# Performance work log

Measured on AMD Instinct MI355X. Metric: run time of the kernel, lower is better.

The kernel has to match this reference:

```python
import jax, jax.numpy as jnp
import numpy as np

S = 4  # HMM states
# allowed transitions among the 4 recurrent states (plus self-loops);
# the (0,4) edge targets a terminal state outside the recurrent block and is omitted
_allow = np.zeros((S, S), dtype=bool)
for i, j in [(0, 0), (1, 1), (2, 2), (3, 3), (0, 1), (1, 2), (2, 3), (0, 2), (1, 3)]:
    _allow[i, j] = True
MASK = jnp.asarray(_allow)
NEG = -1e9


def setup_inputs() -> dict:
    key = jax.random.key(0)
    k0, k1, k2, k3, k4 = jax.random.split(key, 5)
    return {
        "x": jax.random.normal(k0, (256, 4096, 26), dtype=jnp.float32),
        "emit_logits": jax.random.normal(k1, (S, 26), dtype=jnp.float32) * 0.3,
        "trans_logits": jax.random.normal(k2, (S, S), dtype=jnp.float32) * 0.3,
        "init_logits": jax.random.normal(k3, (S,), dtype=jnp.float32) * 0.3,
        "w_out": jax.random.normal(k4, (1, S, 5), dtype=jnp.float32) * 0.3,
    }


def _posterior(x, emit_logits, trans_logits, init_logits):
    # x: [B,T,A] logits -> softmax over alphabet (as in call())
    p = jax.nn.softmax(x, axis=-1)                       # [B,T,A]
    Bmat = jax.nn.softmax(emit_logits, axis=-1)          # [S,A] emission distributions
    # expected emission likelihood per state, in log space
    log_emit = jnp.log(jnp.einsum('bta,sa->bts', p, Bmat) + 1e-16)  # [B,T,S]

    neg = jnp.asarray(NEG, x.dtype)
    logA = jax.nn.log_softmax(jnp.where(MASK, trans_logits, neg), axis=-1)
    logA = jnp.where(MASK, logA, neg)                    # [S,S]
    log_pi = jax.nn.log_softmax(init_logits)             # [S]

    le = jnp.moveaxis(log_emit, 1, 0)                    # [T,B,S]
    T = le.shape[0]

    # forward recursion: alpha_t = e_t + LSE_prev(alpha_{t-1} + logA)
    a0 = log_pi[None, :] + le[0]                         # [B,S]
    def fstep(carry, e):
        nc = e + jax.nn.logsumexp(carry[:, :, None] + logA[None], axis=1)
        return nc, nc
    _, alphas = jax.lax.scan(fstep, a0, le[1:])
    alphas = jnp.concatenate([a0[None], alphas], axis=0)  # [T,B,S]

    # backward recursion: beta_t = LSE_next(logA + e_{t+1} + beta_{t+1})
    bT = jnp.zeros_like(a0)
    def bstep(carry, e_next):
        nc = jax.nn.logsumexp(logA[None] + (e_next + carry)[:, None, :], axis=2)
        return nc, nc
    _, betas = jax.lax.scan(bstep, bT, le[1:], reverse=True)
    betas = jnp.concatenate([betas, bT[None]], axis=0)    # [T,B,S]

    gamma = jax.nn.softmax(alphas + betas, axis=-1)       # posterior [T,B,S]
    return jnp.moveaxis(gamma, 0, 1)[:, :, None, :]       # [B,T,1,S]


def reference(x, emit_logits, trans_logits, init_logits, w_out):
    gamma = _posterior(x, emit_logits, trans_logits, init_logits)  # [B,T,1,S]
    return jnp.einsum('bthd,hdo->bto', gamma, w_out)               # [B,T,5]
```

## Files before the change

### kernel.cpp

```cpp
#include <hip/hip_runtime.h>

#define TDIM 4096
#define BDIM 256
#define ADIM 26
#define SDIM 4
#define NEGF -1e30f
#define LOG2E 1.44269504088896340736f

__device__ __forceinline__ float ex2(float x) { return __builtin_amdgcn_exp2f(x); }
__device__ __forceinline__ float lg2(float x) { return __builtin_amdgcn_logf(x); }

__device__ __forceinline__ float l2se2(float a, float b) {
    float mx = fmaxf(a, b), mn = fminf(a, b);
    return mx + lg2(1.f + ex2(mn - mx));
}
__device__ __forceinline__ float l2se3(float a, float b, float c) {
    float mx = fmaxf(fmaxf(a, b), c);
    float md = __builtin_amdgcn_fmed3f(a, b, c);
    float mn = fminf(fminf(a, b), c);
    return mx + lg2(1.f + ex2(md - mx) + ex2(mn - mx));
}
__device__ __forceinline__ float l2se4(float a, float b, float c, float d) {
    float h1 = fmaxf(a, b), l1 = fminf(a, b);
    float h2 = fmaxf(c, d), l2 = fminf(c, d);
    float mx = fmaxf(h1, h2), s2 = fminf(h1, h2);
    return mx + lg2(1.f + ex2(s2 - mx) + ex2(l1 - mx) + ex2(l2 - mx));
}

struct TransA { float A00, A01, A02, A11, A12, A13, A22, A23, A33; };

__device__ __forceinline__ TransA make_transA(const float* __restrict__ trans) {
    TransA A;
    {
        float l0 = trans[0], l1 = trans[1], l2 = trans[2];
        float m = fmaxf(fmaxf(l0, l1), l2);
        float lz = m + __logf(__expf(l0 - m) + __expf(l1 - m) + __expf(l2 - m));
        A.A00 = (l0 - lz) * LOG2E; A.A01 = (l1 - lz) * LOG2E; A.A02 = (l2 - lz) * LOG2E;
    }
    {
        float l1 = trans[5], l2 = trans[6], l3 = trans[7];
        float m = fmaxf(fmaxf(l1, l2), l3);
        float lz = m + __logf(__expf(l1 - m) + __expf(l2 - m) + __expf(l3 - m));
        A.A11 = (l1 - lz) * LOG2E; A.A12 = (l2 - lz) * LOG2E; A.A13 = (l3 - lz) * LOG2E;
    }
    {
        float l2 = trans[10], l3 = trans[11];
        float m = fmaxf(l2, l3);
        float lz = m + __logf(__expf(l2 - m) + __expf(l3 - m));
        A.A22 = (l2 - lz) * LOG2E; A.A23 = (l3 - lz) * LOG2E;
    }
    A.A33 = 0.f;
    return A;
}

struct UT { float m00, m01, m02, m03, m11, m12, m13, m22, m23, m33; };

__device__ __forceinline__ void fstep(UT& M, const TransA& A, float4 e) {
    float n00 = M.m00 + A.A00 + e.x;
    float n01 = l2se2(M.m00 + A.A01, M.m01 + A.A11) + e.y;
    float n02 = l2se3(M.m00 + A.A02, M.m01 + A.A12, M.m02 + A.A22) + e.z;
    float n03 = l2se3(M.m01 + A.A13, M.m02 + A.A23, M.m03) + e.w;
    float n11 = M.m11 + A.A11 + e.y;
    float n12 = l2se2(M.m11 + A.A12, M.m12 + A.A22) + e.z;
    float n13 = l2se3(M.m11 + A.A13, M.m12 + A.A23, M.m13) + e.w;
    float n22 = M.m22 + A.A22 + e.z;
    float n23 = l2se2(M.m22 + A.A23, M.m23) + e.w;
    float n33 = M.m33 + e.w;
    M.m00 = n00; M.m01 = n01; M.m02 = n02; M.m03 = n03;
    M.m11 = n11; M.m12 = n12; M.m13 = n13; M.m22 = n22; M.m23 = n23; M.m33 = n33;
}

__device__ __forceinline__ UT ut_compose(const UT& A, const UT& B) {
    UT C;
    C.m00 = A.m00 + B.m00;
    C.m01 = l2se2(A.m00 + B.m01, A.m01 + B.m11);
    C.m02 = l2se3(A.m00 + B.m02, A.m01 + B.m12, A.m02 + B.m22);
    C.m03 = l2se4(A.m00 + B.m03, A.m01 + B.m13, A.m02 + B.m23, A.m03 + B.m33);
    C.m11 = A.m11 + B.m11;
    C.m12 = l2se2(A.m11 + B.m12, A.m12 + B.m22);
    C.m13 = l2se3(A.m11 + B.m13, A.m12 + B.m23, A.m13 + B.m33);
    C.m22 = A.m22 + B.m22;
    C.m23 = l2se2(A.m22 + B.m23, A.m23 + B.m33);
    C.m33 = A.m33 + B.m33;
    return C;
}

__device__ __forceinline__ void ut_renorm(UT& M) {
    float m1 = fmaxf(fmaxf(M.m00, M.m01), fmaxf(M.m02, M.m03));
    float m2 = fmaxf(fmaxf(M.m11, M.m12), fmaxf(M.m13, M.m22));
    float m3 = fmaxf(M.m23, M.m33);
    float mx = fmaxf(fmaxf(m1, m2), m3);
    M.m00 -= mx; M.m01 -= mx; M.m02 -= mx; M.m03 -= mx;
    M.m11 -= mx; M.m12 -= mx; M.m13 -= mx; M.m22 -= mx; M.m23 -= mx; M.m33 -= mx;
}

__device__ __forceinline__ void ut_store11(float* p, const UT& M) {
    p[0] = M.m00; p[1] = M.m01; p[2] = M.m02; p[3] = M.m03;
    p[4] = M.m11; p[5] = M.m12; p[6] = M.m13;
    p[7] = M.m22; p[8] = M.m23; p[9] = M.m33;
}
__device__ __forceinline__ UT ut_load11(const float* p) {
    UT M;
    M.m00 = p[0]; M.m01 = p[1]; M.m02 = p[2]; M.m03 = p[3];
    M.m11 = p[4]; M.m12 = p[5]; M.m13 = p[6];
    M.m22 = p[7]; M.m23 = p[8]; M.m33 = p[9];
    return M;
}

__device__ __forceinline__ void vecmat(float& v0, float& v1, float& v2, float& v3,
                                       const float* m) {
    float n0 = v0 + m[0];
    float n1 = l2se2(v0 + m[1], v1 + m[4]);
    float n2 = l2se3(v0 + m[2], v1 + m[5], v2 + m[7]);
    float n3 = l2se4(v0 + m[3], v1 + m[6], v2 + m[8], v3 + m[9]);
    float mm = fmaxf(fmaxf(n0, n1), fmaxf(n2, n3));
    v0 = n0 - mm; v1 = n1 - mm; v2 = n2 - mm; v3 = n3 - mm;
}
__device__ __forceinline__ void matvec(const float* m,
                                       float& u0, float& u1, float& u2, float& u3) {
    float n0 = l2se4(m[0] + u0, m[1] + u1, m[2] + u2, m[3] + u3);
    float n1 = l2se3(m[4] + u1, m[5] + u2, m[6] + u3);
    float n2 = l2se2(m[7] + u2, m[8] + u3);
    float n3 = m[9] + u3;
    float mm = fmaxf(fmaxf(n0, n1), fmaxf(n2, n3));
    u0 = n0 - mm; u1 = n1 - mm; u2 = n2 - mm; u3 = n3 - mm;
}

#define ASTEP(E) do { \
    float4 _e = (E); \
    float n0_ = a0 + A.A00; \
    float n1_ = l2se2(a0 + A.A01, a1 + A.A11); \
    float n2_ = l2se3(a0 + A.A02, a1 + A.A12, a2 + A.A22); \
    float n3_ = l2se3(a1 + A.A13, a2 + A.A23, a3); \
    a0 = n0_ + _e.x; a1 = n1_ + _e.y; a2 = n2_ + _e.z; a3 = n3_ + _e.w; \
    float mm_ = fmaxf(fmaxf(a0, a1), fmaxf(a2, a3)); \
    a0 -= mm_; a1 -= mm_; a2 -= mm_; a3 -= mm_; \
} while (0)

#define BSTEP(E) do { \
    float4 _e = (E); \
    float f0_ = _e.x + b0, f1_ = _e.y + b1, f2_ = _e.z + b2, f3_ = _e.w + b3; \
    float n0_ = l2se3(A.A00 + f0_, A.A01 + f1_, A.A02 + f2_); \
    float n1_ = l2se3(A.A11 + f1_, A.A12 + f2_, A.A13 + f3_); \
    float n2_ = l2se2(A.A22 + f2_, A.A23 + f3_); \
    float n3_ = f3_; \
    float bm_ = fmaxf(fmaxf(n0_, n1_), fmaxf(n2_, n3_)); \
    b0 = n0_ - bm_; b1 = n1_ - bm_; b2 = n2_ - bm_; b3 = n3_ - bm_; \
} while (0)

#define GEMIT(AV, Q) do { \
    float g0_ = (AV).x + b0, g1_ = (AV).y + b1, g2_ = (AV).z + b2, g3_ = (AV).w + b3; \
    float gm_ = fmaxf(fmaxf(g0_, g1_), fmaxf(g2_, g3_)); \
    float q0_ = ex2(g0_ - gm_), q1_ = ex2(g1_ - gm_); \
    float q2_ = ex2(g2_ - gm_), q3_ = ex2(g3_ - gm_); \
    float inv_ = 1.f / (q0_ + q1_ + q2_ + q3_); \
    q0_ *= inv_; q1_ *= inv_; q2_ *= inv_; q3_ *= inv_; \
    vals[(Q)*5 + 0] = fmaf(q0_, wv[0][0], fmaf(q1_, wv[1][0], fmaf(q2_, wv[2][0], q3_ * wv[3][0]))); \
    vals[(Q)*5 + 1] = fmaf(q0_, wv[0][1], fmaf(q1_, wv[1][1], fmaf(q2_, wv[2][1], q3_ * wv[3][1]))); \
    vals[(Q)*5 + 2] = fmaf(q0_, wv[0][2], fmaf(q1_, wv[1][2], fmaf(q2_, wv[2][2], q3_ * wv[3][2]))); \
    vals[(Q)*5 + 3] = fmaf(q0_, wv[0][3], fmaf(q1_, wv[1][3], fmaf(q2_, wv[2][3], q3_ * wv[3][3]))); \
    vals[(Q)*5 + 4] = fmaf(q0_, wv[0][4], fmaf(q1_, wv[1][4], fmaf(q2_, wv[2][4], q3_ * wv[3][4]))); \
} while (0)

#define RDLE(T) sle[(((T) & 31) * 129) + ((T) >> 5)]

#define L0F 0
#define L0B 1408
#define L1F 2816
#define L1B 3520
#define L2F 4224
#define L2B 4576
#define SF  4928
#define SB  5056

__global__ __launch_bounds__(256, 1)
void fused_kernel(const float* __restrict__ x, const float* __restrict__ emit,
                  const float* __restrict__ trans, const float* __restrict__ initl,
                  const float* __restrict__ w, float* __restrict__ out) {
    __shared__ float4 sle[32 * 129];
    __shared__ float4 uni[4352];
    __shared__ float Bmat[SDIM][ADIM];

    float* U = reinterpret_cast<float*>(uni);
    float4* abuf = uni;
    float4* bbuf = uni + 2176;

    const int tid = threadIdx.x;
    const int bidb = blockIdx.x;

    if (tid < SDIM) {
        float m = -1e30f;
        #pragma unroll
        for (int a = 0; a < ADIM; ++a) m = fmaxf(m, emit[tid * ADIM + a]);
        float tmp[ADIM];
        float z = 0.f;
        #pragma unroll
        for (int a = 0; a < ADIM; ++a) {
            float e = __expf(emit[tid * ADIM + a] - m);
            tmp[a] = e; z += e;
        }
        float inv = 1.f / z;
        #pragma unroll
        for (int a = 0; a < ADIM; ++a) Bmat[tid][a] = tmp[a] * inv;
    }
    TransA A = make_transA(trans);
    __syncthreads();

    {
        const float4* xbase = reinterpret_cast<const float4*>(x) + (size_t)bidb * 2048 * 13;
        #pragma unroll 1
        for (int i = 0; i < 8; ++i) {
            const float4* xp = xbase + ((size_t)(i * 256 + tid)) * 13;
            float4 buf[13];
            #pragma unroll
            for (int q = 0; q < 13; ++q) buf[q] = xp[q];

            float d00 = 0.f, d01 = 0.f, d02 = 0.f, d03 = 0.f;
            float d10 = 0.f, d11 = 0.f, d12 = 0.f, d13 = 0.f;
            #pragma unroll
            for (int q = 0; q < 13; ++q) {
                float4 u = buf[q];
                #pragma unroll
                for (int j = 0; j < 4; ++j) {
                    const int e = q * 4 + j;
                    float val = (j == 0) ? u.x : (j == 1) ? u.y : (j == 2) ? u.z : u.w;
                    float ev = ex2(val * LOG2E);
                    if (e < ADIM) {
                        d00 = fmaf(ev, Bmat[0][e], d00); d01 = fmaf(ev, Bmat[1][e], d01);
                        d02 = fmaf(ev, Bmat[2][e], d02); d03 = fmaf(ev, Bmat[3][e], d03);
                    } else {
                        const int a = e - ADIM;
                        d10 = fmaf(ev, Bmat[0][a], d10); d11 = fmaf(ev, Bmat[1][a], d11);
                        d12 = fmaf(ev, Bmat[2][a], d12); d13 = fmaf(ev, Bmat[3][a], d13);
                    }
                }
            }
            float4 r0, r1;
            r0.x = lg2(d00); r0.y = lg2(d01); r0.z = lg2(d02); r0.w = lg2(d03);
            r1.x = lg2(d10); r1.y = lg2(d11); r1.z = lg2(d12); r1.w = lg2(d13);
            int t = (i * 256 + tid) << 1;
            RDLE(t) = r0;
            RDLE(t + 1) = r1;
        }
    }
    __syncthreads();

    const int c = tid & 127;
    const int t0 = c * 32;
    const bool isB = tid >= 128;

    {
        UT M;
        if (!isB) {
            float4 e0 = RDLE(t0);
            if (c == 0) {
                M.m00 = e0.x; M.m11 = e0.y; M.m22 = e0.z; M.m33 = e0.w;
                M.m01 = NEGF; M.m02 = NEGF; M.m03 = NEGF; M.m12 = NEGF; M.m13 = NEGF; M.m23 = NEGF;
            } else {
                M.m00 = A.A00 + e0.x; M.m01 = A.A01 + e0.y; M.m02 = A.A02 + e0.z; M.m03 = NEGF;
                M.m11 = A.A11 + e0.y; M.m12 = A.A12 + e0.z; M.m13 = A.A13 + e0.w;
                M.m22 = A.A22 + e0.z; M.m23 = A.A23 + e0.w; M.m33 = e0.w;
            }
            #pragma unroll 1
            for (int k = 1; k < 32; ++k) fstep(M, A, RDLE(t0 + k));
            ut_renorm(M);
            ut_store11(U + L0F + c * 11, M);
        } else {
            M.m00 = 0.f; M.m11 = 0.f; M.m22 = 0.f; M.m33 = 0.f;
            M.m01 = NEGF; M.m02 = NEGF; M.m03 = NEGF; M.m12 = NEGF; M.m13 = NEGF; M.m23 = NEGF;
            int nst = (c == 127) ? 31 : 32;
            #pragma unroll 1
            for (int k = 0; k < nst; ++k) fstep(M, A, RDLE(t0 + 1 + k));
            ut_renorm(M);
            ut_store11(U + L0B + c * 11, M);
        }
    }
    __syncthreads();

    if (tid < 128) {
        int dir = tid >> 6;
        int i = tid & 63;
        const float* src = U + (dir ? L0B : L0F);
        float* dst = U + (dir ? L1B : L1F);
        UT P = ut_compose(ut_load11(src + (2 * i) * 11), ut_load11(src + (2 * i + 1) * 11));
        ut_renorm(P);
        ut_store11(dst + i * 11, P);
    }
    __syncthreads();

    if (tid < 64) {
        int dir = tid >> 5;
        int i = tid & 31;
        const float* src = U + (dir ? L1B : L1F);
        float* dst = U + (dir ? L2B : L2F);
        UT P = ut_compose(ut_load11(src + (2 * i) * 11), ut_load11(src + (2 * i + 1) * 11));
        ut_renorm(P);
        ut_store11(dst + i * 11, P);
    }
    __syncthreads();

    if (tid == 0) {
        float i0 = initl[0], i1 = initl[1], i2 = initl[2], i3 = initl[3];
        float m = fmaxf(fmaxf(i0, i1), fmaxf(i2, i3));
        float lz = m + __logf(__expf(i0 - m) + __expf(i1 - m) + __expf(i2 - m) + __expf(i3 - m));
        float v0 = (i0 - lz) * LOG2E, v1 = (i1 - lz) * LOG2E;
        float v2 = (i2 - lz) * LOG2E, v3 = (i3 - lz) * LOG2E;
        #pragma unroll 1
        for (int g = 0; g < 32; ++g) {
            U[SF + g * 4 + 0] = v0; U[SF + g * 4 + 1] = v1;
            U[SF + g * 4 + 2] = v2; U[SF + g * 4 + 3] = v3;
            vecmat(v0, v1, v2, v3, U + L2F + g * 11);
        }
    } else if (tid == 64) {
        float u0 = 0.f, u1 = 0.f, u2 = 0.f, u3 = 0.f;
        #pragma unroll 1
        for (int g = 31; g >= 0; --g) {
            U[SB + g * 4 + 0] = u0; U[SB + g * 4 + 1] = u1;
            U[SB + g * 4 + 2] = u2; U[SB + g * 4 + 3] = u3;
            matvec(U + L2B + g * 11, u0, u1, u2, u3);
        }
    }
    __syncthreads();

    float fa0, fa1, fa2, fa3;
    float fb0, fb1, fb2, fb3;
    {
        int g = c >> 2, r = c & 3;
        if (!isB) {
            fa0 = U[SF + g * 4 + 0]; fa1 = U[SF + g * 4 + 1];
            fa2 = U[SF + g * 4 + 2]; fa3 = U[SF + g * 4 + 3];
            if (r >= 2) vecmat(fa0, fa1, fa2, fa3, U + L1F + (2 * g) * 11);
            if (r & 1)  vecmat(fa0, fa1, fa2, fa3, U + L0F + (c - 1) * 11);
        } else {
            fb0 = U[SB + g * 4 + 0]; fb1 = U[SB + g * 4 + 1];
            fb2 = U[SB + g * 4 + 2]; fb3 = U[SB + g * 4 + 3];
            if (r <= 1)       matvec(U + L1B + (2 * g + 1) * 11, fb0, fb1, fb2, fb3);
            if ((r & 1) == 0) matvec(U + L0B + (c + 1) * 11, fb0, fb1, fb2, fb3);
        }
    }
    __syncthreads();

    float wv[SDIM][5];
    #pragma unroll
    for (int s = 0; s < SDIM; ++s)
        #pragma unroll
        for (int o = 0; o < 5; ++o) wv[s][o] = w[s * 5 + o];

    float* opb = out + (size_t)bidb * TDIM * 5;
    float vals[20];

    if (!isB) {
        float a0 = fa0, a1 = fa1, a2 = fa2, a3 = fa3;
        if (c == 0) {
            float4 e = RDLE(0);
            a0 += e.x; a1 += e.y; a2 += e.z; a3 += e.w;
            float mm = fmaxf(fmaxf(a0, a1), fmaxf(a2, a3));
            a0 -= mm; a1 -= mm; a2 -= mm; a3 -= mm;
        } else {
            ASTEP(RDLE(t0));
        }
        abuf[c * 17 + 0] = make_float4(a0, a1, a2, a3);
        #pragma unroll 1
        for (int k = 1; k < 16; ++k) {
            ASTEP(RDLE(t0 + k));
            abuf[c * 17 + k] = make_float4(a0, a1, a2, a3);
        }
        __syncthreads();
        float b0, b1, b2, b3;
        #pragma unroll 1
        for (int g = 4; g < 8; ++g) {
            #pragma unroll
            for (int q = 0; q < 4; ++q) {
                int k = g * 4 + q;
                ASTEP(RDLE(t0 + k));
                float4 bv = bbuf[c * 17 + (k - 16)];
                b0 = bv.x; b1 = bv.y; b2 = bv.z; b3 = bv.w;
                float4 av = make_float4(a0, a1, a2, a3);
                GEMIT(av, q);
            }
            float4* vo = reinterpret_cast<float4*>(opb + (size_t)(t0 + g * 4) * 5);
            vo[0] = make_float4(vals[0],  vals[1],  vals[2],  vals[3]);
            vo[1] = make_float4(vals[4],  vals[5],  vals[6],  vals[7]);
            vo[2] = make_float4(vals[8],  vals[9],  vals[10], vals[11]);
            vo[3] = make_float4(vals[12], vals[13], vals[14], vals[15]);
            vo[4] = make_float4(vals[16], vals[17], vals[18], vals[19]);
        }
    } else {
        float b0 = fb0, b1 = fb1, b2 = fb2, b3 = fb3;
        bool lastc = (c == 127);
        #pragma unroll 1
        for (int k = 31; k >= 16; --k) {
            if (!(lastc && k == 31)) BSTEP(RDLE(t0 + 1 + k));
            bbuf[c * 17 + (k - 16)] = make_float4(b0, b1, b2, b3);
        }
        __syncthreads();
        #pragma unroll 1
        for (int g = 3; g >= 0; --g) {
            #pragma unroll
            for (int q = 3; q >= 0; --q) {
                int k = g * 4 + q;
                BSTEP(RDLE(t0 + 1 + k));
                float4 av = abuf[c * 17 + k];
                GEMIT(av, q);
            }
            float4* vo = reinterpret_cast<float4*>(opb + (size_t)(t0 + g * 4) * 5);
            vo[0] = make_float4(vals[0],  vals[1],  vals[2],  vals[3]);
            vo[1] = make_float4(vals[4],  vals[5],  vals[6],  vals[7]);
            vo[2] = make_float4(vals[8],  vals[9],  vals[10], vals[11]);
            vo[3] = make_float4(vals[12], vals[13], vals[14], vals[15]);
            vo[4] = make_float4(vals[16], vals[17], vals[18], vals[19]);
        }
    }
}

extern "C" void kernel_launch(void* const* d_in, const int* in_sizes, int n_in,
                              void* d_out, int out_size, void* d_ws, size_t ws_size,
                              hipStream_t stream) {
    const float* x     = (const float*)d_in[0];
    const float* emit  = (const float*)d_in[1];
    const float* trans = (const float*)d_in[2];
    const float* initl = (const float*)d_in[3];
    const float* w     = (const float*)d_in[4];
    float* out = (float*)d_out;

    hipLaunchKernelGGL(fused_kernel, dim3(BDIM), dim3(256), 0, stream,
                       x, emit, trans, initl, w, out);
}
```

Measured before the change: 48.35 us.

## Double threads per block and shorten per-thread HMM chunks with extra scan level

Doubles the block to 512 threads so each forward/backward thread handles 16 time steps instead of 32, which shortens the serial recursion chains. An extra level is added to the tree composition of transfer matrices, and the chunk-prefix reconstruction now uses three levels. The shared-memory layouts for the emission buffer and the alpha/beta buffers are reindexed to stay conflict-free. This adds one more barrier-separated reduction stage and more shared-memory use per block, in exchange for twice the parallelism across each sequence.

```diff
diff --git a/kernel.cpp b/kernel.cpp
--- a/kernel.cpp
+++ b/kernel.cpp
@@ -162,28 +162,30 @@
     vals[(Q)*5 + 4] = fmaf(q0_, wv[0][4], fmaf(q1_, wv[1][4], fmaf(q2_, wv[2][4], q3_ * wv[3][4]))); \
 } while (0)
 
-#define RDLE(T) sle[(((T) & 31) * 129) + ((T) >> 5)]
+#define RDLE(T) sle[(((T) & 15) * 257) + ((T) >> 4)]
 
 #define L0F 0
-#define L0B 1408
-#define L1F 2816
-#define L1B 3520
-#define L2F 4224
-#define L2B 4576
-#define SF  4928
-#define SB  5056
-
-__global__ __launch_bounds__(256, 1)
+#define L0B 2816
+#define L1F 5632
+#define L1B 7040
+#define L2F 8448
+#define L2B 9152
+#define L3F 9856
+#define L3B 10208
+#define SF  10560
+#define SB  10688
+
+__global__ __launch_bounds__(512, 1)
 void fused_kernel(const float* __restrict__ x, const float* __restrict__ emit,
                   const float* __restrict__ trans, const float* __restrict__ initl,
                   const float* __restrict__ w, float* __restrict__ out) {
-    __shared__ float4 sle[32 * 129];
-    __shared__ float4 uni[4352];
+    __shared__ float4 sle[16 * 257];
+    __shared__ float4 uni[4096];
     __shared__ float Bmat[SDIM][ADIM];
 
     float* U = reinterpret_cast<float*>(uni);
     float4* abuf = uni;
-    float4* bbuf = uni + 2176;
+    float4* bbuf = uni + 2048;
 
     const int tid = threadIdx.x;
     const int bidb = blockIdx.x;
@@ -209,8 +211,8 @@
     {
         const float4* xbase = reinterpret_cast<const float4*>(x) + (size_t)bidb * 2048 * 13;
         #pragma unroll 1
-        for (int i = 0; i < 8; ++i) {
-            const float4* xp = xbase + ((size_t)(i * 256 + tid)) * 13;
+        for (int i = 0; i < 4; ++i) {
+            const float4* xp = xbase + ((size_t)(i * 512 + tid)) * 13;
             float4 buf[13];
             #pragma unroll
             for (int q = 0; q < 13; ++q) buf[q] = xp[q];
@@ -238,16 +240,16 @@
             float4 r0, r1;
             r0.x = lg2(d00); r0.y = lg2(d01); r0.z = lg2(d02); r0.w = lg2(d03);
             r1.x = lg2(d10); r1.y = lg2(d11); r1.z = lg2(d12); r1.w = lg2(d13);
-            int t = (i * 256 + tid) << 1;
+            int t = (i * 512 + tid) << 1;
             RDLE(t) = r0;
             RDLE(t + 1) = r1;
         }
     }
     __syncthreads();
 
-    const int c = tid & 127;
-    const int t0 = c * 32;
-    const bool isB = tid >= 128;
+    const int c = tid & 255;
+    const int t0 = c * 16;
+    const bool isB = tid >= 256;
 
     {
         UT M;
@@ -262,13 +264,13 @@
                 M.m22 = A.A22 + e0.z; M.m23 = A.A23 + e0.w; M.m33 = e0.w;
             }
             #pragma unroll 1
-            for (int k = 1; k < 32; ++k) fstep(M, A, RDLE(t0 + k));
+            for (int k = 1; k < 16; ++k) fstep(M, A, RDLE(t0 + k));
             ut_renorm(M);
             ut_store11(U + L0F + c * 11, M);
         } else {
             M.m00 = 0.f; M.m11 = 0.f; M.m22 = 0.f; M.m33 = 0.f;
             M.m01 = NEGF; M.m02 = NEGF; M.m03 = NEGF; M.m12 = NEGF; M.m13 = NEGF; M.m23 = NEGF;
-            int nst = (c == 127) ? 31 : 32;
+            int nst = (c == 255) ? 15 : 16;
             #pragma unroll 1
             for (int k = 0; k < nst; ++k) fstep(M, A, RDLE(t0 + 1 + k));
             ut_renorm(M);
@@ -277,9 +279,9 @@
     }
     __syncthreads();
 
-    if (tid < 128) {
-        int dir = tid >> 6;
-        int i = tid & 63;
+    if (tid < 256) {
+        int dir = tid >> 7;
+        int i = tid & 127;
         const float* src = U + (dir ? L0B : L0F);
         float* dst = U + (dir ? L1B : L1F);
         UT P = ut_compose(ut_load11(src + (2 * i) * 11), ut_load11(src + (2 * i + 1) * 11));
@@ -288,11 +290,22 @@
     }
     __syncthreads();
 
+    if (tid < 128) {
+        int dir = tid >> 6;
+        int i = tid & 63;
+        const float* src = U + (dir ? L1B : L1F);
+        float* dst = U + (dir ? L2B : L2F);
+        UT P = ut_compose(ut_load11(src + (2 * i) * 11), ut_load11(src + (2 * i + 1) * 11));
+        ut_renorm(P);
+        ut_store11(dst + i * 11, P);
+    }
+    __syncthreads();
+
     if (tid < 64) {
         int dir = tid >> 5;
         int i = tid & 31;
-        const float* src = U + (dir ? L1B : L1F);
-        float* dst = U + (dir ? L2B : L2F);
+        const float* src = U + (dir ? L2B : L2F);
+        float* dst = U + (dir ? L3B : L3F);
         UT P = ut_compose(ut_load11(src + (2 * i) * 11), ut_load11(src + (2 * i + 1) * 11));
         ut_renorm(P);
         ut_store11(dst + i * 11, P);
@@ -309,7 +322,7 @@
         for (int g = 0; g < 32; ++g) {
             U[SF + g * 4 + 0] = v0; U[SF + g * 4 + 1] = v1;
             U[SF + g * 4 + 2] = v2; U[SF + g * 4 + 3] = v3;
-            vecmat(v0, v1, v2, v3, U + L2F + g * 11);
+            vecmat(v0, v1, v2, v3, U + L3F + g * 11);
         }
     } else if (tid == 64) {
         float u0 = 0.f, u1 = 0.f, u2 = 0.f, u3 = 0.f;
@@ -317,7 +330,7 @@
         for (int g = 31; g >= 0; --g) {
             U[SB + g * 4 + 0] = u0; U[SB + g * 4 + 1] = u1;
             U[SB + g * 4 + 2] = u2; U[SB + g * 4 + 3] = u3;
-            matvec(U + L2B + g * 11, u0, u1, u2, u3);
+            matvec(U + L3B + g * 11, u0, u1, u2, u3);
         }
     }
     __syncthreads();
@@ -325,17 +338,19 @@
     float fa0, fa1, fa2, fa3;
     float fb0, fb1, fb2, fb3;
     {
-        int g = c >> 2, r = c & 3;
+        int g = c >> 3;
         if (!isB) {
             fa0 = U[SF + g * 4 + 0]; fa1 = U[SF + g * 4 + 1];
             fa2 = U[SF + g * 4 + 2]; fa3 = U[SF + g * 4 + 3];
-            if (r >= 2) vecmat(fa0, fa1, fa2, fa3, U + L1F + (2 * g) * 11);
-            if (r & 1)  vecmat(fa0, fa1, fa2, fa3, U + L0F + (c - 1) * 11);
+            if (c & 4) vecmat(fa0, fa1, fa2, fa3, U + L2F + (2 * g) * 11);
+            if (c & 2) vecmat(fa0, fa1, fa2, fa3, U + L1F + ((c >> 2) * 2) * 11);
+            if (c & 1) vecmat(fa0, fa1, fa2, fa3, U + L0F + (c - 1) * 11);
         } else {
             fb0 = U[SB + g * 4 + 0]; fb1 = U[SB + g * 4 + 1];
             fb2 = U[SB + g * 4 + 2]; fb3 = U[SB + g * 4 + 3];
-            if (r <= 1)       matvec(U + L1B + (2 * g + 1) * 11, fb0, fb1, fb2, fb3);
-            if ((r & 1) == 0) matvec(U + L0B + (c + 1) * 11, fb0, fb1, fb2, fb3);
+            if (!(c & 4)) matvec(U + L2B + (2 * g + 1) * 11, fb0, fb1, fb2, fb3);
+            if (!(c & 2)) matvec(U + L1B + ((c >> 2) * 2 + 1) * 11, fb0, fb1, fb2, fb3);
+            if (!(c & 1)) matvec(U + L0B + (c + 1) * 11, fb0, fb1, fb2, fb3);
         }
     }
     __syncthreads();
@@ -359,26 +374,26 @@
         } else {
             ASTEP(RDLE(t0));
         }
-        abuf[c * 17 + 0] = make_float4(a0, a1, a2, a3);
-        #pragma unroll 1
-        for (int k = 1; k < 16; ++k) {
+        abuf[0 * 256 + c] = make_float4(a0, a1, a2, a3);
+        #pragma unroll 1
+        for (int k = 1; k < 8; ++k) {
             ASTEP(RDLE(t0 + k));
-            abuf[c * 17 + k] = make_float4(a0, a1, a2, a3);
+            abuf[k * 256 + c] = make_float4(a0, a1, a2, a3);
         }
         __syncthreads();
         float b0, b1, b2, b3;
         #pragma unroll 1
-        for (int g = 4; g < 8; ++g) {
+        for (int g2 = 0; g2 < 2; ++g2) {
             #pragma unroll
             for (int q = 0; q < 4; ++q) {
-                int k = g * 4 + q;
+                int k = 8 + g2 * 4 + q;
                 ASTEP(RDLE(t0 + k));
-                float4 bv = bbuf[c * 17 + (k - 16)];
+                float4 bv = bbuf[(k - 8) * 256 + c];
                 b0 = bv.x; b1 = bv.y; b2 = bv.z; b3 = bv.w;
                 float4 av = make_float4(a0, a1, a2, a3);
                 GEMIT(av, q);
             }
-            float4* vo = reinterpret_cast<float4*>(opb + (size_t)(t0 + g * 4) * 5);
+            float4* vo = reinterpret_cast<float4*>(opb + (size_t)(t0 + 8 + g2 * 4) * 5);
             vo[0] = make_float4(vals[0],  vals[1],  vals[2],  vals[3]);
             vo[1] = make_float4(vals[4],  vals[5],  vals[6],  vals[7]);
             vo[2] = make_float4(vals[8],  vals[9],  vals[10], vals[11]);
@@ -387,23 +402,23 @@
         }
     } else {
         float b0 = fb0, b1 = fb1, b2 = fb2, b3 = fb3;
-        bool lastc = (c == 127);
-        #pragma unroll 1
-        for (int k = 31; k >= 16; --k) {
-            if (!(lastc && k == 31)) BSTEP(RDLE(t0 + 1 + k));
-            bbuf[c * 17 + (k - 16)] = make_float4(b0, b1, b2, b3);
+        bool lastc = (c == 255);
+        #pragma unroll 1
+        for (int k = 15; k >= 8; --k) {
+            if (!(lastc && k == 15)) BSTEP(RDLE(t0 + 1 + k));
+            bbuf[(k - 8) * 256 + c] = make_float4(b0, b1, b2, b3);
         }
         __syncthreads();
         #pragma unroll 1
-        for (int g = 3; g >= 0; --g) {
+        for (int g2 = 1; g2 >= 0; --g2) {
             #pragma unroll
             for (int q = 3; q >= 0; --q) {
-                int k = g * 4 + q;
+                int k = g2 * 4 + q;
                 BSTEP(RDLE(t0 + 1 + k));
-                float4 av = abuf[c * 17 + k];
+                float4 av = abuf[k * 256 + c];
                 GEMIT(av, q);
             }
-            float4* vo = reinterpret_cast<float4*>(opb + (size_t)(t0 + g * 4) * 5);
+            float4* vo = reinterpret_cast<float4*>(opb + (size_t)(t0 + g2 * 4) * 5);
             vo[0] = make_float4(vals[0],  vals[1],  vals[2],  vals[3]);
             vo[1] = make_float4(vals[4],  vals[5],  vals[6],  vals[7]);
             vo[2] = make_float4(vals[8],  vals[9],  vals[10], vals[11]);
@@ -423,6 +438,6 @@
     const float* w     = (const float*)d_in[4];
     float* out = (float*)d_out;
 
-    hipLaunchKernelGGL(fused_kernel, dim3(BDIM), dim3(256), 0, stream,
+    hipLaunchKernelGGL(fused_kernel, dim3(BDIM), dim3(512), 0, stream,
                        x, emit, trans, initl, w, out);
 }
```

After: 47.50 us. Within noise of the previous version (-1.8%).
